# Performance work log

Hardware: AMD Instinct MI355X
Metric: run time of the kernel (lower is better)

Reference implementation:

```python
import jax, jax.numpy as jnp
import numpy as np

B, T, C, F = 512, 1024, 8, 8
ISIZE = C * F  # 64
OSIZE = 64


def setup_inputs() -> dict:
    key = jax.random.key(0)
    k_x, k_w, k_b = jax.random.split(key, 3)
    x = jax.random.normal(k_x, (B, T, C, F), dtype=jnp.float32)
    # per-group Linear params, torch nn.Linear layout: weight [osize, isize], bias [osize]
    bound = 1.0 / np.sqrt(ISIZE)
    W = jax.random.uniform(k_w, (T, OSIZE, ISIZE), dtype=jnp.float32, minval=-bound, maxval=bound)
    b = jax.random.uniform(k_b, (T, OSIZE), dtype=jnp.float32, minval=-bound, maxval=bound)
    return {"x": x, "W": W, "b": b}


def reference(x, W, b):
    # collapseDims: cat(x.split(1, 2), 3).squeeze(2) == reshape [B,T,C,F] -> [B,T,C*F]
    Bn, Tn, Cn, Fn = x.shape
    xc = x.reshape(Bn, Tn, Cn * Fn)
    # per-slice Linear along dim=1 (T groups): y[b,t,:] = xc[b,t,:] @ W[t].T + b[t]
    out = jnp.einsum("bti,toi->bto", xc, W) + b[None, :, :]
    return out
```

## Files before the change

kernel.cpp:

```cpp
#include <hip/hip_runtime.h>


#define T_DIM 1024
#define B_DIM 512
#define KSZ 64
#define OSZ 64
#define ROWS 64
#define PITCH 68

__global__ __launch_bounds__(256, 4) void pl_kernel(
    const float* __restrict__ x,
    const float* __restrict__ W,
    const float* __restrict__ bias,
    float* __restrict__ out)
{
    __shared__ float Wt[KSZ * PITCH];
    __shared__ float Xs[ROWS * PITCH];

    const int t     = blockIdx.x >> 3;
    const int chunk = blockIdx.x & 7;
    const int row0  = chunk * ROWS;
    const int tid   = threadIdx.x;

    const float4* Wg = (const float4*)(W + (size_t)t * (OSZ * KSZ));
    #pragma unroll
    for (int j = 0; j < 4; ++j) {
        int idx = tid + j * 256;
        int o   = idx >> 4;
        int i0  = (idx & 15) << 2;
        float4 wv = Wg[idx];
        Wt[(i0 + 0) * PITCH + o] = wv.x;
        Wt[(i0 + 1) * PITCH + o] = wv.y;
        Wt[(i0 + 2) * PITCH + o] = wv.z;
        Wt[(i0 + 3) * PITCH + o] = wv.w;
    }

    #pragma unroll
    for (int it = 0; it < 4; ++it) {
        int r  = (tid >> 4) + it * 16;
        int i0 = (tid & 15) << 2;
        const float4* xg = (const float4*)(x + ((size_t)(row0 + r) * T_DIM + t) * KSZ + i0);
        float4 xv = *xg;
        *(float4*)&Xs[r * PITCH + i0] = xv;
    }

    __syncthreads();

    const int tr = tid >> 4;
    const int tc = tid & 15;

    float acc[4][4] = {};

    #pragma unroll 8
    for (int i = 0; i < KSZ; ++i) {
        float4 wv = *(const float4*)&Wt[i * PITCH + (tc << 2)];
        float xk0 = Xs[(tr * 4 + 0) * PITCH + i];
        float xk1 = Xs[(tr * 4 + 1) * PITCH + i];
        float xk2 = Xs[(tr * 4 + 2) * PITCH + i];
        float xk3 = Xs[(tr * 4 + 3) * PITCH + i];
        acc[0][0] += xk0 * wv.x; acc[0][1] += xk0 * wv.y; acc[0][2] += xk0 * wv.z; acc[0][3] += xk0 * wv.w;
        acc[1][0] += xk1 * wv.x; acc[1][1] += xk1 * wv.y; acc[1][2] += xk1 * wv.z; acc[1][3] += xk1 * wv.w;
        acc[2][0] += xk2 * wv.x; acc[2][1] += xk2 * wv.y; acc[2][2] += xk2 * wv.z; acc[2][3] += xk2 * wv.w;
        acc[3][0] += xk3 * wv.x; acc[3][1] += xk3 * wv.y; acc[3][2] += xk3 * wv.z; acc[3][3] += xk3 * wv.w;
    }

    float4 bv = *(const float4*)(bias + (size_t)t * OSZ + (tc << 2));
    #pragma unroll
    for (int k = 0; k < 4; ++k) {
        int b = row0 + tr * 4 + k;
        float4 res;
        res.x = acc[k][0] + bv.x;
        res.y = acc[k][1] + bv.y;
        res.z = acc[k][2] + bv.z;
        res.w = acc[k][3] + bv.w;
        *(float4*)(out + ((size_t)b * T_DIM + t) * OSZ + (tc << 2)) = res;
    }
}

extern "C" void kernel_launch(void* const* d_in, const int* in_sizes, int n_in,
                              void* d_out, int out_size, void* d_ws, size_t ws_size,
                              hipStream_t stream) {
    const float* x    = (const float*)d_in[0];
    const float* W    = (const float*)d_in[1];
    const float* bias = (const float*)d_in[2];
    float* out        = (float*)d_out;

    dim3 grid(T_DIM * (B_DIM / ROWS));
    dim3 block(256);
    pl_kernel<<<grid, block, 0, stream>>>(x, W, bias, out);
}
```

Baseline: 77.84 us.

## Enlarge row tile to 256 with 8x8 register blocking and swizzled transposed X

Each block now handles 256 batch rows per group instead of 64, so W is loaded and transposed into LDS once per 256 rows, and each thread computes an 8x8 output tile from float4 LDS reads. X is stored transposed in LDS with an XOR swizzle so the inner loop can use vector loads without bank conflicts. The larger tile raises register and LDS use (launch bounds drop to 2 blocks per CU) and cuts the grid to 2048 blocks, which lowers occupancy and latency hiding for what is mainly a memory-bound kernel.

Result: slower. 83.30 us (+7.0%).

```diff
diff --git a/kernel.cpp b/kernel.cpp
--- a/kernel.cpp
+++ b/kernel.cpp
@@ -5,75 +5,95 @@
 #define B_DIM 512
 #define KSZ 64
 #define OSZ 64
-#define ROWS 64
-#define PITCH 68
+#define ROWS 256
 
-__global__ __launch_bounds__(256, 4) void pl_kernel(
+__global__ __launch_bounds__(256, 2) void pl_kernel(
     const float* __restrict__ x,
     const float* __restrict__ W,
     const float* __restrict__ bias,
     float* __restrict__ out)
 {
-    __shared__ float Wt[KSZ * PITCH];
-    __shared__ float Xs[ROWS * PITCH];
+    __shared__ float Xs[KSZ * ROWS];
+    __shared__ float Wt[KSZ * OSZ];
 
-    const int t     = blockIdx.x >> 3;
-    const int chunk = blockIdx.x & 7;
+    const int t     = blockIdx.x >> 1;
+    const int chunk = blockIdx.x & 1;
     const int row0  = chunk * ROWS;
     const int tid   = threadIdx.x;
 
-    const float4* Wg = (const float4*)(W + (size_t)t * (OSZ * KSZ));
-    #pragma unroll
-    for (int j = 0; j < 4; ++j) {
-        int idx = tid + j * 256;
-        int o   = idx >> 4;
-        int i0  = (idx & 15) << 2;
-        float4 wv = Wg[idx];
-        Wt[(i0 + 0) * PITCH + o] = wv.x;
-        Wt[(i0 + 1) * PITCH + o] = wv.y;
-        Wt[(i0 + 2) * PITCH + o] = wv.z;
-        Wt[(i0 + 3) * PITCH + o] = wv.w;
+    {
+        const int o  = tid & 63;
+        const int ib = (tid >> 6) << 4;
+        const float* wg = W + (size_t)t * (OSZ * KSZ) + (size_t)o * KSZ + ib;
+        #pragma unroll
+        for (int c = 0; c < 4; ++c) {
+            float4 wv = *(const float4*)(wg + 4 * c);
+            Wt[(ib + 4 * c + 0) * OSZ + o] = wv.x;
+            Wt[(ib + 4 * c + 1) * OSZ + o] = wv.y;
+            Wt[(ib + 4 * c + 2) * OSZ + o] = wv.z;
+            Wt[(ib + 4 * c + 3) * OSZ + o] = wv.w;
+        }
     }
 
-    #pragma unroll
-    for (int it = 0; it < 4; ++it) {
-        int r  = (tid >> 4) + it * 16;
-        int i0 = (tid & 15) << 2;
-        const float4* xg = (const float4*)(x + ((size_t)(row0 + r) * T_DIM + t) * KSZ + i0);
-        float4 xv = *xg;
-        *(float4*)&Xs[r * PITCH + i0] = xv;
+    {
+        const int g = tid >> 4;
+        const int q = tid & 15;
+        #pragma unroll
+        for (int it = 0; it < 4; ++it) {
+            const int r0 = 64 * it + 4 * g;
+            const float* xg = x + ((size_t)(row0 + r0) * T_DIM + t) * KSZ + 4 * q;
+            float4 a0 = *(const float4*)(xg);
+            float4 a1 = *(const float4*)(xg + (size_t)T_DIM * KSZ);
+            float4 a2 = *(const float4*)(xg + 2 * (size_t)T_DIM * KSZ);
+            float4 a3 = *(const float4*)(xg + 3 * (size_t)T_DIM * KSZ);
+            float4 v0 = make_float4(a0.x, a1.x, a2.x, a3.x);
+            float4 v1 = make_float4(a0.y, a1.y, a2.y, a3.y);
+            float4 v2 = make_float4(a0.z, a1.z, a2.z, a3.z);
+            float4 v3 = make_float4(a0.w, a1.w, a2.w, a3.w);
+            const int gsw = (((16 * it + g) ^ (q & 7)) << 2);
+            *(float4*)&Xs[(4 * q + 0) * ROWS + gsw] = v0;
+            *(float4*)&Xs[(4 * q + 1) * ROWS + gsw] = v1;
+            *(float4*)&Xs[(4 * q + 2) * ROWS + gsw] = v2;
+            *(float4*)&Xs[(4 * q + 3) * ROWS + gsw] = v3;
+        }
     }
 
     __syncthreads();
 
-    const int tr = tid >> 4;
-    const int tc = tid & 15;
+    const int tr = tid >> 3;
+    const int tc = tid & 7;
 
-    float acc[4][4] = {};
+    float acc[8][8] = {};
 
-    #pragma unroll 8
+    #pragma unroll 4
     for (int i = 0; i < KSZ; ++i) {
-        float4 wv = *(const float4*)&Wt[i * PITCH + (tc << 2)];
-        float xk0 = Xs[(tr * 4 + 0) * PITCH + i];
-        float xk1 = Xs[(tr * 4 + 1) * PITCH + i];
-        float xk2 = Xs[(tr * 4 + 2) * PITCH + i];
-        float xk3 = Xs[(tr * 4 + 3) * PITCH + i];
-        acc[0][0] += xk0 * wv.x; acc[0][1] += xk0 * wv.y; acc[0][2] += xk0 * wv.z; acc[0][3] += xk0 * wv.w;
-        acc[1][0] += xk1 * wv.x; acc[1][1] += xk1 * wv.y; acc[1][2] += xk1 * wv.z; acc[1][3] += xk1 * wv.w;
-        acc[2][0] += xk2 * wv.x; acc[2][1] += xk2 * wv.y; acc[2][2] += xk2 * wv.z; acc[2][3] += xk2 * wv.w;
-        acc[3][0] += xk3 * wv.x; acc[3][1] += xk3 * wv.y; acc[3][2] += xk3 * wv.z; acc[3][3] += xk3 * wv.w;
+        const int f = (i >> 2) & 7;
+        float4 xa = *(const float4*)&Xs[i * ROWS + (((2 * tr)     ^ f) << 2)];
+        float4 xb = *(const float4*)&Xs[i * ROWS + (((2 * tr + 1) ^ f) << 2)];
+        float4 wa = *(const float4*)&Wt[i * OSZ + 8 * tc];
+        float4 wb = *(const float4*)&Wt[i * OSZ + 8 * tc + 4];
+        float xs[8] = {xa.x, xa.y, xa.z, xa.w, xb.x, xb.y, xb.z, xb.w};
+        float ws[8] = {wa.x, wa.y, wa.z, wa.w, wb.x, wb.y, wb.z, wb.w};
+        #pragma unroll
+        for (int r = 0; r < 8; ++r)
+            #pragma unroll
+            for (int c = 0; c < 8; ++c)
+                acc[r][c] += xs[r] * ws[c];
     }
 
-    float4 bv = *(const float4*)(bias + (size_t)t * OSZ + (tc << 2));
+    float4 bv0 = *(const float4*)(bias + (size_t)t * OSZ + 8 * tc);
+    float4 bv1 = *(const float4*)(bias + (size_t)t * OSZ + 8 * tc + 4);
     #pragma unroll
-    for (int k = 0; k < 4; ++k) {
-        int b = row0 + tr * 4 + k;
-        float4 res;
-        res.x = acc[k][0] + bv.x;
-        res.y = acc[k][1] + bv.y;
-        res.z = acc[k][2] + bv.z;
-        res.w = acc[k][3] + bv.w;
-        *(float4*)(out + ((size_t)b * T_DIM + t) * OSZ + (tc << 2)) = res;
+    for (int r = 0; r < 8; ++r) {
+        const size_t b = (size_t)row0 + 8 * tr + r;
+        float* op = out + (b * T_DIM + t) * OSZ + 8 * tc;
+        float4 o0, o1;
+        o0.x = acc[r][0] + bv0.x; o0.y = acc[r][1] + bv0.y;
+        o0.z = acc[r][2] + bv0.z; o0.w = acc[r][3] + bv0.w;
+        o1.x = acc[r][4] + bv1.x; o1.y = acc[r][5] + bv1.y;
+        o1.z = acc[r][6] + bv1.z; o1.w = acc[r][7] + bv1.w;
+        *(float4*)(op)     = o0;
+        *(float4*)(op + 4) = o1;
     }
 }
 
```

## Keep per-lane weight rows in registers and stream wave-uniform x rows

Applied to the files above, without the earlier changes.

Replaces the LDS-tiled GEMM with one block per group t, where each lane holds one output's 64 weights in registers and each wave streams 128 batch rows, reading x with wave-uniform addresses. Packed two-wide FMAs do the dot products, and each output row is written as one coalesced store. This drops the LDS staging, transposes and barriers. In exchange it relies on uniform (possibly scalar) loads for x, cuts the grid to 1024 blocks and raises register pressure.

Result: slower. 213.6 us (+174.5%).

```diff
diff --git a/kernel.cpp b/kernel.cpp
--- a/kernel.cpp
+++ b/kernel.cpp
@@ -5,8 +5,8 @@
 #define B_DIM 512
 #define KSZ 64
 #define OSZ 64
-#define ROWS 64
-#define PITCH 68
+
+typedef float v2 __attribute__((ext_vector_type(2)));
 
 __global__ __launch_bounds__(256, 4) void pl_kernel(
     const float* __restrict__ x,
@@ -14,66 +14,50 @@
     const float* __restrict__ bias,
     float* __restrict__ out)
 {
-    __shared__ float Wt[KSZ * PITCH];
-    __shared__ float Xs[ROWS * PITCH];
+    const int t    = blockIdx.x;
+    const int tid  = threadIdx.x;
+    const int lane = tid & 63;
+    const int wv   = __builtin_amdgcn_readfirstlane(tid >> 6);
 
-    const int t     = blockIdx.x >> 3;
-    const int chunk = blockIdx.x & 7;
-    const int row0  = chunk * ROWS;
-    const int tid   = threadIdx.x;
+    v2 w2[32];
+    {
+        const float* wp = W + (size_t)t * (OSZ * KSZ) + (size_t)lane * KSZ;
+        #pragma unroll
+        for (int j = 0; j < 16; ++j) {
+            float4 wv4 = *(const float4*)(wp + 4 * j);
+            w2[2 * j + 0][0] = wv4.x; w2[2 * j + 0][1] = wv4.y;
+            w2[2 * j + 1][0] = wv4.z; w2[2 * j + 1][1] = wv4.w;
+        }
+    }
+    const float bv = bias[(size_t)t * OSZ + lane];
 
-    const float4* Wg = (const float4*)(W + (size_t)t * (OSZ * KSZ));
-    #pragma unroll
-    for (int j = 0; j < 4; ++j) {
-        int idx = tid + j * 256;
-        int o   = idx >> 4;
-        int i0  = (idx & 15) << 2;
-        float4 wv = Wg[idx];
-        Wt[(i0 + 0) * PITCH + o] = wv.x;
-        Wt[(i0 + 1) * PITCH + o] = wv.y;
-        Wt[(i0 + 2) * PITCH + o] = wv.z;
-        Wt[(i0 + 3) * PITCH + o] = wv.w;
-    }
+    const size_t rstride = (size_t)T_DIM * KSZ;
 
-    #pragma unroll
-    for (int it = 0; it < 4; ++it) {
-        int r  = (tid >> 4) + it * 16;
-        int i0 = (tid & 15) << 2;
-        const float4* xg = (const float4*)(x + ((size_t)(row0 + r) * T_DIM + t) * KSZ + i0);
-        float4 xv = *xg;
-        *(float4*)&Xs[r * PITCH + i0] = xv;
-    }
+    for (int c = 0; c < 16; ++c) {
+        const int r0 = wv * 128 + c * 8;
+        const float* xp = x + ((size_t)r0 * T_DIM + t) * KSZ;
 
-    __syncthreads();
+        v2 acc[8];
+        #pragma unroll
+        for (int r = 0; r < 8; ++r) { acc[r][0] = 0.f; acc[r][1] = 0.f; }
 
-    const int tr = tid >> 4;
-    const int tc = tid & 15;
+        #pragma unroll
+        for (int ib = 0; ib < 16; ++ib) {
+            #pragma unroll
+            for (int r = 0; r < 8; ++r) {
+                float4 xv = *(const float4*)(xp + (size_t)r * rstride + 4 * ib);
+                v2 xa; xa[0] = xv.x; xa[1] = xv.y;
+                v2 xb; xb[0] = xv.z; xb[1] = xv.w;
+                acc[r] = __builtin_elementwise_fma(xa, w2[2 * ib + 0], acc[r]);
+                acc[r] = __builtin_elementwise_fma(xb, w2[2 * ib + 1], acc[r]);
+            }
+        }
 
-    float acc[4][4] = {};
-
-    #pragma unroll 8
-    for (int i = 0; i < KSZ; ++i) {
-        float4 wv = *(const float4*)&Wt[i * PITCH + (tc << 2)];
-        float xk0 = Xs[(tr * 4 + 0) * PITCH + i];
-        float xk1 = Xs[(tr * 4 + 1) * PITCH + i];
-        float xk2 = Xs[(tr * 4 + 2) * PITCH + i];
-        float xk3 = Xs[(tr * 4 + 3) * PITCH + i];
-        acc[0][0] += xk0 * wv.x; acc[0][1] += xk0 * wv.y; acc[0][2] += xk0 * wv.z; acc[0][3] += xk0 * wv.w;
-        acc[1][0] += xk1 * wv.x; acc[1][1] += xk1 * wv.y; acc[1][2] += xk1 * wv.z; acc[1][3] += xk1 * wv.w;
-        acc[2][0] += xk2 * wv.x; acc[2][1] += xk2 * wv.y; acc[2][2] += xk2 * wv.z; acc[2][3] += xk2 * wv.w;
-        acc[3][0] += xk3 * wv.x; acc[3][1] += xk3 * wv.y; acc[3][2] += xk3 * wv.z; acc[3][3] += xk3 * wv.w;
-    }
-
-    float4 bv = *(const float4*)(bias + (size_t)t * OSZ + (tc << 2));
-    #pragma unroll
-    for (int k = 0; k < 4; ++k) {
-        int b = row0 + tr * 4 + k;
-        float4 res;
-        res.x = acc[k][0] + bv.x;
-        res.y = acc[k][1] + bv.y;
-        res.z = acc[k][2] + bv.z;
-        res.w = acc[k][3] + bv.w;
-        *(float4*)(out + ((size_t)b * T_DIM + t) * OSZ + (tc << 2)) = res;
+        #pragma unroll
+        for (int r = 0; r < 8; ++r) {
+            out[((size_t)(r0 + r) * T_DIM + t) * OSZ + lane] =
+                acc[r][0] + acc[r][1] + bv;
+        }
     }
 }
 
@@ -85,7 +69,7 @@
     const float* bias = (const float*)d_in[2];
     float* out        = (float*)d_out;
 
-    dim3 grid(T_DIM * (B_DIM / ROWS));
+    dim3 grid(T_DIM);
     dim3 block(256);
     pl_kernel<<<grid, block, 0, stream>>>(x, W, bias, out);
 }
```
